# Performance work log

Hardware: AMD Instinct MI355X
Metric: run time of the kernel (lower is better)

The kernel has to match this reference:

```python
import jax, jax.numpy as jnp
import numpy as np


def setup_inputs() -> dict:
    key = jax.random.key(0)
    k1, k2, k3, k4 = jax.random.split(key, 4)
    B, Cin, Cout, K, Wd, H, Wsp = 16, 256, 256, 3, 256, 64, 64
    fan_in = Cin * K * K
    return {
        "x": jax.random.normal(k1, (B, Cin, H, Wsp), dtype=jnp.float32),
        "w": jax.random.normal(k2, (B, Wd), dtype=jnp.float32),
        "conv_weight": jax.random.normal(k3, (Cout, Cin, K, K), dtype=jnp.float32) * 0.05,
        "style_w": jax.random.normal(k4, (Cin, Wd), dtype=jnp.float32) * 0.05,
        "style_b": jnp.zeros((Cin,), dtype=jnp.float32),
        "scale": jnp.asarray(1.0 / np.sqrt(fan_in), dtype=jnp.float32),
    }


def reference(x, w, conv_weight, style_w, style_b, scale):
    # x: [B, Cin, H, W]; w: [B, Wd]; conv_weight: [Cout, Cin, K, K]
    B, Cin, H, Wsp = x.shape
    Cout, _, K, _ = conv_weight.shape
    # style modulation: s = Linear(w) -> [B, 1, Cin, 1, 1]
    s = (w @ style_w.T + style_b).reshape(B, 1, Cin, 1, 1)
    # modulate + demodulate per-sample weights: [B, Cout, Cin, K, K]
    wt = (conv_weight * scale)[None] * s
    demod = jax.lax.rsqrt(jnp.sum(wt * wt, axis=(2, 3, 4), keepdims=True) + 1e-8)
    wt = (wt * demod).reshape(B * Cout, Cin, K, K)
    # grouped conv emulation: input [1, B*Cin, H, W], groups=B
    xr = x.reshape(1, B * Cin, H, Wsp)
    pad = 1
    out = jax.lax.conv_general_dilated(
        xr, wt,
        window_strides=(1, 1),
        padding=[(pad, pad), (pad, pad)],
        dimension_numbers=("NCHW", "OIHW", "NCHW"),
        feature_group_count=B,
    )
    return out.reshape(B, Cout, out.shape[2], out.shape[3])
```

## Files before the change

kernel.cpp:

```cpp
#include <hip/hip_runtime.h>
#include <hip/hip_bf16.h>

#define BB   16
#define CIN  256
#define COUT 256
#define WD   256
#define HH   64
#define WWS  64
#define NSP  4096
#define KW   9

typedef __attribute__((ext_vector_type(8))) short short8;
typedef __attribute__((ext_vector_type(4))) float f32x4;
typedef unsigned short ushort_t;
typedef unsigned int uint_t;

#define S_BYTES (BB*CIN*4)
#define WT_OFF (S_BYTES)
#define WT_BYTES (BB*9*COUT*CIN*2)
#define X_OFF (WT_OFF + WT_BYTES)
#define X_BYTES (BB*NSP*CIN*2)
#define ZP_OFF (X_OFF + X_BYTES)
#define ZP_BYTES 4096
#define WS_NEEDED ((size_t)(ZP_OFF + ZP_BYTES))

#define WAITVM0 asm volatile("s_waitcnt vmcnt(0)" ::: "memory")
#define WAITVM4 asm volatile("s_waitcnt vmcnt(4)" ::: "memory")

__device__ inline ushort_t f2bf(float f) {
    __hip_bfloat16 h = __float2bfloat16(f);
    return __builtin_bit_cast(ushort_t, h);
}

__device__ inline void gload_lds16(const ushort_t* g, ushort_t* l) {
    __builtin_amdgcn_global_load_lds(
        (const __attribute__((address_space(1))) void*)g,
        (__attribute__((address_space(3))) void*)l, 16, 0, 0);
}

__global__ __launch_bounds__(256)
void style_kernel(const float* __restrict__ w,
                  const float* __restrict__ style_w,
                  const float* __restrict__ style_b,
                  float* __restrict__ s) {
    const int b  = blockIdx.x;
    const int ci = threadIdx.x;
    __shared__ float wsh[WD];
    wsh[ci] = w[b * WD + ci];
    __syncthreads();
    const float* row = style_w + ci * WD;
    float acc = style_b[ci];
    #pragma unroll 4
    for (int k = 0; k < WD; ++k) acc += wsh[k] * row[k];
    s[b * CIN + ci] = acc;
}

__global__ __launch_bounds__(256)
void wt_kernel(const float* __restrict__ cw, const float* __restrict__ s,
               const float* __restrict__ scale_p, ushort_t* __restrict__ wt,
               float* __restrict__ zp) {
    const int co = blockIdx.x, b = blockIdx.y, ci = threadIdx.x;
    if (co == 0 && b == 0)
        ((float4*)zp)[ci] = make_float4(0.f, 0.f, 0.f, 0.f);
    const float sv = s[b * CIN + ci] * scale_p[0];
    const float* cp = cw + ((size_t)co * CIN + ci) * KW;
    float v[9];
    float ss = 0.f;
    #pragma unroll
    for (int t = 0; t < 9; ++t) { v[t] = cp[t] * sv; ss += v[t] * v[t]; }
    #pragma unroll
    for (int off = 32; off > 0; off >>= 1) ss += __shfl_down(ss, off);
    __shared__ float red[4];
    if ((ci & 63) == 0) red[ci >> 6] = ss;
    __syncthreads();
    const float dm = rsqrtf(red[0] + red[1] + red[2] + red[3] + 1e-8f);
    #pragma unroll
    for (int t = 0; t < 9; ++t)
        wt[((size_t)(b * 9 + t) * COUT + co) * CIN + ci] = f2bf(v[t] * dm);
}

__global__ __launch_bounds__(256)
void xpose_kernel(const float* __restrict__ x, ushort_t* __restrict__ xo) {
    const int spt = blockIdx.x;
    const int cit = blockIdx.y;
    const int b   = blockIdx.z;
    const int t   = threadIdx.x;
    __shared__ ushort_t tile[64 * 72];
    const int sp0 = spt * 64, ci0 = cit * 64;
    {
        const int spq = t & 15, cil = t >> 4;
        #pragma unroll
        for (int i = 0; i < 4; ++i) {
            const int ci = cil + i * 16;
            const float4 v = *(const float4*)(x + ((size_t)(b * CIN + ci0 + ci)) * NSP + sp0 + spq * 4);
            tile[(spq * 4 + 0) * 72 + ci] = f2bf(v.x);
            tile[(spq * 4 + 1) * 72 + ci] = f2bf(v.y);
            tile[(spq * 4 + 2) * 72 + ci] = f2bf(v.z);
            tile[(spq * 4 + 3) * 72 + ci] = f2bf(v.w);
        }
    }
    __syncthreads();
    {
        const int g8 = t & 7, sp = t >> 3;
        #pragma unroll
        for (int i = 0; i < 2; ++i) {
            const int spp = sp + i * 32;
            uint4 v = *(const uint4*)&tile[spp * 72 + g8 * 8];
            *(uint4*)(xo + ((size_t)(b * NSP + sp0 + spp)) * CIN + ci0 + g8 * 8) = v;
        }
    }
}

__global__ __launch_bounds__(512, 2)
void conv_mfma_kernel(const ushort_t* __restrict__ wt,
                      const ushort_t* __restrict__ xo,
                      const ushort_t* __restrict__ zp,
                      float* __restrict__ out) {
    const int wg    = blockIdx.x;
    const int b     = (wg & 7) | (((wg >> 3) & 1) << 3);
    const int ntile = wg >> 4;
    const int y0    = ntile * 4;

    const int tid  = threadIdx.x;
    const int lane = tid & 63;
    const int w    = tid >> 6;
    const int wm   = w >> 1;
    const int wn   = w & 1;
    const int wn2  = wn * 2;
    const int l15  = lane & 15;
    const int lg   = lane >> 4;

    __shared__ __align__(16) ushort_t lds_x[6 * 66 * 128];

    const ushort_t* pa = wt + (size_t)b * (9 * COUT * CIN)
                       + (uint_t)(wm * 64 + l15) * CIN + (uint_t)(lg * 8);

    const ushort_t* xob = xo + (size_t)b * (NSP * CIN);

    f32x4 acc[4][8];
    #pragma unroll
    for (int mi = 0; mi < 4; ++mi)
        #pragma unroll
        for (int ni = 0; ni < 8; ++ni) acc[mi][ni] = (f32x4){0.f, 0.f, 0.f, 0.f};

    short8 af[2][4];

    if (tid < 192) {
        const int r = tid / 32, rem = tid % 32;
        const int c = (rem & 1) * 65, q2 = rem >> 1;
        *(uint4*)&lds_x[r * 8448 + c * 128 + q2 * 8] = make_uint4(0, 0, 0, 0);
    }

    #define STAGE_X(hh)                                                        \
    {   _Pragma("unroll")                                                      \
        for (int i_ = 0; i_ < 12; ++i_) {                                      \
            const int id_ = w + 8 * i_;                                        \
            const int r_  = id_ >> 4;                                \
            const int cg_ = id_ & 15;                             \
            const int y_  = y0 - 1 + r_;                                       \
            const int colIdx_ = 1 + cg_ * 4 + (lane >> 4);                     \
            const int sq_ = (lane & 15) ^ (colIdx_ & 15);                      \
            const ushort_t* src_ = (y_ >= 0 && y_ < HH)                        \
                ? (xob + (uint_t)(y_ * WWS + cg_ * 4 + (lane >> 4)) * CIN      \
                       + (hh) * 128 + sq_ * 8)                                 \
                : (zp + (lane & 15) * 8);                                      \
            gload_lds16(src_, lds_x + r_ * 8448 + (1 + cg_ * 4) * 128          \
                              + lane * 8);                                     \
        }                                                                      \
    }

    STAGE_X(0);
    #pragma unroll
    for (int mi = 0; mi < 4; ++mi)
        af[0][mi] = *(const short8*)(pa + mi * 4096);
    #pragma unroll
    for (int mi = 0; mi < 4; ++mi)
        af[1][mi] = *(const short8*)(pa + 65536 + mi * 4096);

    WAITVM0;
    asm volatile("s_waitcnt lgkmcnt(0)" ::: "memory");
    __builtin_amdgcn_sched_barrier(0);
    __builtin_amdgcn_s_barrier();

    #define TAP(t, CHPAR, cgv, xcb)                                            \
    {                                                                          \
        WAITVM4;                          \
        __builtin_amdgcn_sched_barrier(0);                                     \
        const int ky_ = (t) / 3, kx_ = (t) % 3;                                \
        const int P_  = ((CHPAR) + (t)) & 1;                                   \
        const ushort_t* bq_ = lds_x + (wn2 + ky_) * 8448 + xcb[kx_];           \
        short8 bf_[8];                                                         \
        _Pragma("unroll")                                                      \
        for (int ni_ = 0; ni_ < 8; ++ni_)                                      \
            bf_[ni_] = *(const short8*)(bq_ + (ni_ >> 2) * 8448                \
                                        + (ni_ & 3) * 2048);                   \
        __builtin_amdgcn_s_setprio(1);                                         \
        _Pragma("unroll")                                                      \
        for (int mi_ = 0; mi_ < 4; ++mi_)                                      \
            _Pragma("unroll")                                                  \
            for (int ni_ = 0; ni_ < 8; ++ni_)                                  \
                acc[mi_][ni_] = __builtin_amdgcn_mfma_f32_16x16x32_bf16(       \
                    bf_[ni_], af[P_][mi_], acc[mi_][ni_], 0, 0, 0);            \
        __builtin_amdgcn_s_setprio(0);                                         \
        __builtin_amdgcn_sched_barrier(0);                                     \
        {                        \
            const int t2_  = ((t) + 2) % 9;                                    \
            const int cg2_ = ((cgv) + (((t) + 2) / 9)) & 7;                    \
            const ushort_t* ap_ = pa + t2_ * 65536 + cg2_ * 32;                \
            _Pragma("unroll")                                                  \
            for (int mi_ = 0; mi_ < 4; ++mi_)                                  \
                af[P_][mi_] = *(const short8*)(ap_ + mi_ * 4096);              \
        }                                                                      \
        __builtin_amdgcn_sched_barrier(0);                                     \
    }

    #define CHUNK9(CHPAR, cgv, clv)                                            \
    {   int xcb[3];                                                            \
        _Pragma("unroll")                                                      \
        for (int kx_ = 0; kx_ < 3; ++kx_) {                                    \
            const int pos_ = ((clv) * 4 + lg) ^ ((l15 + kx_) & 15);            \
            xcb[kx_] = (l15 + kx_) * 128 + pos_ * 8;                           \
        }                                                                      \
        TAP(0, CHPAR, cgv, xcb) TAP(1, CHPAR, cgv, xcb)                        \
        TAP(2, CHPAR, cgv, xcb) TAP(3, CHPAR, cgv, xcb)                        \
        TAP(4, CHPAR, cgv, xcb) TAP(5, CHPAR, cgv, xcb)                        \
        TAP(6, CHPAR, cgv, xcb) TAP(7, CHPAR, cgv, xcb)                        \
        TAP(8, CHPAR, cgv, xcb)                                                \
    }

    #pragma unroll 1
    for (int h = 0; h < 2; ++h) {
        if (h) {
            asm volatile("s_waitcnt lgkmcnt(0)" ::: "memory");
            __builtin_amdgcn_sched_barrier(0);
            __builtin_amdgcn_s_barrier();
            STAGE_X(1);
            WAITVM0;
            __builtin_amdgcn_sched_barrier(0);
            __builtin_amdgcn_s_barrier();
        }
        #pragma unroll 1
        for (int c2 = 0; c2 < 2; ++c2) {
            const int cl0 = c2 * 2;
            const int cg0 = h * 4 + cl0;
            CHUNK9(0, cg0, cl0)
            const int cl1 = c2 * 2 + 1;
            const int cg1 = h * 4 + cl1;
            CHUNK9(1, cg1, cl1)
        }
    }
    #undef TAP
    #undef CHUNK9
    #undef STAGE_X

    asm volatile("s_waitcnt vmcnt(0) lgkmcnt(0)" ::: "memory");
    __builtin_amdgcn_sched_barrier(0);

    #pragma unroll
    for (int mi = 0; mi < 4; ++mi) {
        const int co = wm * 64 + mi * 16 + l15;
        float* ob = out + ((size_t)(b * COUT + co)) * NSP
                  + ntile * 256 + wn * 128 + lg * 4;
        #pragma unroll
        for (int ni = 0; ni < 8; ++ni)
            *(f32x4*)(ob + (ni >> 2) * 64 + (ni & 3) * 16) = acc[mi][ni];
    }
}

__global__ __launch_bounds__(256)
void modconv_kernel(const float* __restrict__ x,
                    const float* __restrict__ cw,
                    const float* __restrict__ s,
                    const float* __restrict__ scale_p,
                    float* __restrict__ out) {
    const int tile = blockIdx.x;
    const int co   = blockIdx.y;
    const int b    = blockIdx.z;
    const int tid  = threadIdx.x;
    const float scale = scale_p[0];

    __shared__ float s_wt[CIN * KW];
    __shared__ float s_x[18 * 66];
    __shared__ float red[4];

    const float* cwb = cw + (size_t)co * CIN * KW;
    const float* sb  = s + b * CIN;
    float sumsq = 0.f;
    for (int i = tid; i < CIN * KW; i += 256) {
        float v = cwb[i] * scale * sb[i / KW];
        s_wt[i] = v;
        sumsq += v * v;
    }
    #pragma unroll
    for (int off = 32; off > 0; off >>= 1) sumsq += __shfl_down(sumsq, off);
    if ((tid & 63) == 0) red[tid >> 6] = sumsq;
    __syncthreads();
    const float demod = rsqrtf(red[0] + red[1] + red[2] + red[3] + 1e-8f);
    for (int i = tid; i < CIN * KW; i += 256) s_wt[i] *= demod;

    const int tx = tid & 63;
    const int tr = tid >> 6;
    const int y0 = tile * 16;
    float acc[4] = {0.f, 0.f, 0.f, 0.f};

    for (int ci = 0; ci < CIN; ++ci) {
        __syncthreads();
        const float* xb = x + ((size_t)(b * CIN + ci)) * (HH * WWS);
        for (int idx = tid; idx < 18 * 66; idx += 256) {
            const int r = idx / 66, c = idx % 66;
            const int yg = y0 - 1 + r, xg = c - 1;
            float v = 0.f;
            if (yg >= 0 && yg < HH && xg >= 0 && xg < WWS) v = xb[yg * WWS + xg];
            s_x[idx] = v;
        }
        __syncthreads();
        const float* wr = s_wt + ci * KW;
        const float w0 = wr[0], w1 = wr[1], w2 = wr[2];
        const float w3 = wr[3], w4 = wr[4], w5 = wr[5];
        const float w6 = wr[6], w7 = wr[7], w8 = wr[8];
        const int rbase = tr * 4;
        float xv[6][3];
        #pragma unroll
        for (int j = 0; j < 6; ++j)
            #pragma unroll
            for (int k = 0; k < 3; ++k) xv[j][k] = s_x[(rbase + j) * 66 + tx + k];
        #pragma unroll
        for (int i = 0; i < 4; ++i)
            acc[i] += w0 * xv[i][0] + w1 * xv[i][1] + w2 * xv[i][2]
                    + w3 * xv[i+1][0] + w4 * xv[i+1][1] + w5 * xv[i+1][2]
                    + w6 * xv[i+2][0] + w7 * xv[i+2][1] + w8 * xv[i+2][2];
    }
    float* ob = out + (((size_t)(b * COUT + co)) * HH + y0) * WWS + tx;
    #pragma unroll
    for (int i = 0; i < 4; ++i) ob[(tr * 4 + i) * WWS] = acc[i];
}

extern "C" void kernel_launch(void* const* d_in, const int* in_sizes, int n_in,
                              void* d_out, int out_size, void* d_ws, size_t ws_size,
                              hipStream_t stream) {
    const float* x       = (const float*)d_in[0];
    const float* w       = (const float*)d_in[1];
    const float* cw      = (const float*)d_in[2];
    const float* style_w = (const float*)d_in[3];
    const float* style_b = (const float*)d_in[4];
    const float* scale_p = (const float*)d_in[5];
    float*       out     = (float*)d_out;

    float*    s    = (float*)d_ws;
    ushort_t* wswt = (ushort_t*)((char*)d_ws + WT_OFF);
    ushort_t* wsx  = (ushort_t*)((char*)d_ws + X_OFF);
    float*    zp   = (float*)((char*)d_ws + ZP_OFF);

    style_kernel<<<dim3(BB), 256, 0, stream>>>(w, style_w, style_b, s);

    if (ws_size >= WS_NEEDED) {
        wt_kernel<<<dim3(COUT, BB), 256, 0, stream>>>(cw, s, scale_p, wswt, zp);
        xpose_kernel<<<dim3(64, 4, BB), 256, 0, stream>>>(x, wsx);
        conv_mfma_kernel<<<dim3(256), 512, 0, stream>>>(wswt, wsx,
                                                        (const ushort_t*)zp, out);
    } else {
        modconv_kernel<<<dim3(4, COUT, BB), 256, 0, stream>>>(x, cw, s, scale_p, out);
    }
}
```

Before: 130.3 us.

## Split conv workgroups across output-channel halves with smaller 64-channel LDS tiles

Each conv workgroup now covers half the output channels with 256 threads instead of all 256 channels with 512 threads. The grid doubles to 512 blocks. The input tile is staged in four 64-channel quarters instead of two 128-channel halves, which halves LDS use and allows more resident blocks per CU. The cost is that every input tile is now loaded twice, once per channel half, and there are more staging barriers per block.

```diff
diff --git a/kernel.cpp b/kernel.cpp
--- a/kernel.cpp
+++ b/kernel.cpp
@@ -111,15 +111,16 @@
     }
 }
 
-__global__ __launch_bounds__(512, 2)
+__global__ __launch_bounds__(256, 2)
 void conv_mfma_kernel(const ushort_t* __restrict__ wt,
                       const ushort_t* __restrict__ xo,
                       const ushort_t* __restrict__ zp,
                       float* __restrict__ out) {
-    const int wg    = blockIdx.x;
-    const int b     = (wg & 7) | (((wg >> 3) & 1) << 3);
-    const int ntile = wg >> 4;
-    const int y0    = ntile * 4;
+    const int wg     = blockIdx.x;
+    const int b      = (wg & 7) | (((wg >> 3) & 1) << 3);
+    const int cohalf = (wg >> 4) & 1;
+    const int ntile  = wg >> 5;
+    const int y0     = ntile * 4;
 
     const int tid  = threadIdx.x;
     const int lane = tid & 63;
@@ -130,11 +131,11 @@
     const int l15  = lane & 15;
     const int lg   = lane >> 4;
 
-    __shared__ __align__(16) ushort_t lds_x[6 * 66 * 128];
+    __shared__ __align__(16) ushort_t lds_x[6 * 66 * 64];
 
     const ushort_t* pa = wt + (size_t)b * (9 * COUT * CIN)
-                       + (uint_t)(wm * 64 + l15) * CIN + (uint_t)(lg * 8);
-
+                       + (uint_t)(cohalf * 128 + wm * 64 + l15) * CIN
+                       + (uint_t)(lg * 8);
     const ushort_t* xob = xo + (size_t)b * (NSP * CIN);
 
     f32x4 acc[4][8];
@@ -145,55 +146,42 @@
 
     short8 af[2][4];
 
-    if (tid < 192) {
-        const int r = tid / 32, rem = tid % 32;
-        const int c = (rem & 1) * 65, q2 = rem >> 1;
-        *(uint4*)&lds_x[r * 8448 + c * 128 + q2 * 8] = make_uint4(0, 0, 0, 0);
-    }
-
-    #define STAGE_X(hh)                                                        \
+    if (tid < 96) {
+        const int cell = tid >> 3;
+        const int r = cell >> 1, c = (cell & 1) * 65;
+        *(uint4*)&lds_x[(r * 66 + c) * 64 + (tid & 7) * 8] =
+            make_uint4(0, 0, 0, 0);
+    }
+
+    #define STAGE_X(qt)                                                        \
     {   _Pragma("unroll")                                                      \
         for (int i_ = 0; i_ < 12; ++i_) {                                      \
-            const int id_ = w + 8 * i_;                                        \
-            const int r_  = id_ >> 4;                                \
-            const int cg_ = id_ & 15;                             \
+            const int cell_ = i_ * 4 + w;                           \
+            const int r_  = cell_ >> 3;                              \
+            const int c0_ = 1 + (cell_ & 7) * 8;                               \
             const int y_  = y0 - 1 + r_;                                       \
-            const int colIdx_ = 1 + cg_ * 4 + (lane >> 4);                     \
-            const int sq_ = (lane & 15) ^ (colIdx_ & 15);                      \
+            const int c_  = c0_ + (lane >> 3);                                 \
+            const int qq_ = (lane & 7) ^ (c_ & 7);                             \
             const ushort_t* src_ = (y_ >= 0 && y_ < HH)                        \
-                ? (xob + (uint_t)(y_ * WWS + cg_ * 4 + (lane >> 4)) * CIN      \
-                       + (hh) * 128 + sq_ * 8)                                 \
-                : (zp + (lane & 15) * 8);                                      \
-            gload_lds16(src_, lds_x + r_ * 8448 + (1 + cg_ * 4) * 128          \
-                              + lane * 8);                                     \
+                ? (xob + (uint_t)(y_ * WWS + c_ - 1) * CIN + (qt) * 64         \
+                       + qq_ * 8)                                              \
+                : (zp + lane * 8);                                             \
+            gload_lds16(src_, lds_x + (r_ * 66 + c0_) * 64 + lane * 8);        \
         }                                                                      \
     }
 
-    STAGE_X(0);
-    #pragma unroll
-    for (int mi = 0; mi < 4; ++mi)
-        af[0][mi] = *(const short8*)(pa + mi * 4096);
-    #pragma unroll
-    for (int mi = 0; mi < 4; ++mi)
-        af[1][mi] = *(const short8*)(pa + 65536 + mi * 4096);
-
-    WAITVM0;
-    asm volatile("s_waitcnt lgkmcnt(0)" ::: "memory");
-    __builtin_amdgcn_sched_barrier(0);
-    __builtin_amdgcn_s_barrier();
-
-    #define TAP(t, CHPAR, cgv, xcb)                                            \
+    #define TAPB(ch2, t, BX, PAQ, PAQN)                                        \
     {                                                                          \
-        WAITVM4;                          \
+        constexpr int u_ = (ch2) * 9 + (t);                                    \
+        constexpr int P_ = u_ & 1;                                             \
+        WAITVM4;                                                               \
         __builtin_amdgcn_sched_barrier(0);                                     \
-        const int ky_ = (t) / 3, kx_ = (t) % 3;                                \
-        const int P_  = ((CHPAR) + (t)) & 1;                                   \
-        const ushort_t* bq_ = lds_x + (wn2 + ky_) * 8448 + xcb[kx_];           \
+        constexpr int ky_ = (t) / 3, kx_ = (t) % 3;                            \
         short8 bf_[8];                                                         \
         _Pragma("unroll")                                                      \
         for (int ni_ = 0; ni_ < 8; ++ni_)                                      \
-            bf_[ni_] = *(const short8*)(bq_ + (ni_ >> 2) * 8448                \
-                                        + (ni_ & 3) * 2048);                   \
+            bf_[ni_] = *(const short8*)(lds_x + BX[kx_]                        \
+                        + (((ni_ >> 2) + ky_) * 66) * 64 + (ni_ & 3) * 1024);  \
         __builtin_amdgcn_s_setprio(1);                                         \
         _Pragma("unroll")                                                      \
         for (int mi_ = 0; mi_ < 4; ++mi_)                                      \
@@ -204,9 +192,15 @@
         __builtin_amdgcn_s_setprio(0);                                         \
         __builtin_amdgcn_sched_barrier(0);                                     \
         {                        \
-            const int t2_  = ((t) + 2) % 9;                                    \
-            const int cg2_ = ((cgv) + (((t) + 2) / 9)) & 7;                    \
-            const ushort_t* ap_ = pa + t2_ * 65536 + cg2_ * 32;                \
+            const ushort_t* ap_;                                               \
+            if constexpr (u_ + 2 < 18) {                                       \
+                constexpr int tap2_ = (u_ + 2) % 9;                            \
+                constexpr int cgo_  = (u_ + 2) / 9;                            \
+                ap_ = (PAQ) + tap2_ * 65536 + cgo_ * 32;                       \
+            } else {                                                           \
+                constexpr int tap2_ = u_ - 16;                                 \
+                ap_ = (PAQN) + tap2_ * 65536;                                  \
+            }                                                                  \
             _Pragma("unroll")                                                  \
             for (int mi_ = 0; mi_ < 4; ++mi_)                                  \
                 af[P_][mi_] = *(const short8*)(ap_ + mi_ * 4096);              \
@@ -214,43 +208,49 @@
         __builtin_amdgcn_sched_barrier(0);                                     \
     }
 
-    #define CHUNK9(CHPAR, cgv, clv)                                            \
-    {   int xcb[3];                                                            \
-        _Pragma("unroll")                                                      \
-        for (int kx_ = 0; kx_ < 3; ++kx_) {                                    \
-            const int pos_ = ((clv) * 4 + lg) ^ ((l15 + kx_) & 15);            \
-            xcb[kx_] = (l15 + kx_) * 128 + pos_ * 8;                           \
-        }                                                                      \
-        TAP(0, CHPAR, cgv, xcb) TAP(1, CHPAR, cgv, xcb)                        \
-        TAP(2, CHPAR, cgv, xcb) TAP(3, CHPAR, cgv, xcb)                        \
-        TAP(4, CHPAR, cgv, xcb) TAP(5, CHPAR, cgv, xcb)                        \
-        TAP(6, CHPAR, cgv, xcb) TAP(7, CHPAR, cgv, xcb)                        \
-        TAP(8, CHPAR, cgv, xcb)                                                \
-    }
+    STAGE_X(0);
+    #pragma unroll
+    for (int mi = 0; mi < 4; ++mi)
+        af[0][mi] = *(const short8*)(pa + mi * 4096);
+    #pragma unroll
+    for (int mi = 0; mi < 4; ++mi)
+        af[1][mi] = *(const short8*)(pa + 65536 + mi * 4096);
+    WAITVM0;
+    asm volatile("s_waitcnt lgkmcnt(0)" ::: "memory");
+    __builtin_amdgcn_sched_barrier(0);
+    __builtin_amdgcn_s_barrier();
 
     #pragma unroll 1
-    for (int h = 0; h < 2; ++h) {
-        if (h) {
+    for (int qt = 0; qt < 4; ++qt) {
+        if (qt) {
             asm volatile("s_waitcnt lgkmcnt(0)" ::: "memory");
             __builtin_amdgcn_sched_barrier(0);
             __builtin_amdgcn_s_barrier();
-            STAGE_X(1);
+            STAGE_X(qt);
             WAITVM0;
             __builtin_amdgcn_sched_barrier(0);
             __builtin_amdgcn_s_barrier();
         }
-        #pragma unroll 1
-        for (int c2 = 0; c2 < 2; ++c2) {
-            const int cl0 = c2 * 2;
-            const int cg0 = h * 4 + cl0;
-            CHUNK9(0, cg0, cl0)
-            const int cl1 = c2 * 2 + 1;
-            const int cg1 = h * 4 + cl1;
-            CHUNK9(1, cg1, cl1)
-        }
-    }
-    #undef TAP
-    #undef CHUNK9
+        const ushort_t* paq  = pa + qt * 64;
+        const ushort_t* paqn = pa + ((qt + 1) & 3) * 64;
+
+        int bx0[3], bx1[3];
+        #pragma unroll
+        for (int kx = 0; kx < 3; ++kx) {
+            const int colb = (wn2 * 66 + l15 + kx) * 64;
+            const int k7   = (l15 + kx) & 7;
+            bx0[kx] = colb + ((0 + lg) ^ k7) * 8;
+            bx1[kx] = colb + ((4 + lg) ^ k7) * 8;
+        }
+
+        TAPB(0,0,bx0,paq,paqn) TAPB(0,1,bx0,paq,paqn) TAPB(0,2,bx0,paq,paqn)
+        TAPB(0,3,bx0,paq,paqn) TAPB(0,4,bx0,paq,paqn) TAPB(0,5,bx0,paq,paqn)
+        TAPB(0,6,bx0,paq,paqn) TAPB(0,7,bx0,paq,paqn) TAPB(0,8,bx0,paq,paqn)
+        TAPB(1,0,bx1,paq,paqn) TAPB(1,1,bx1,paq,paqn) TAPB(1,2,bx1,paq,paqn)
+        TAPB(1,3,bx1,paq,paqn) TAPB(1,4,bx1,paq,paqn) TAPB(1,5,bx1,paq,paqn)
+        TAPB(1,6,bx1,paq,paqn) TAPB(1,7,bx1,paq,paqn) TAPB(1,8,bx1,paq,paqn)
+    }
+    #undef TAPB
     #undef STAGE_X
 
     asm volatile("s_waitcnt vmcnt(0) lgkmcnt(0)" ::: "memory");
@@ -258,7 +258,7 @@
 
     #pragma unroll
     for (int mi = 0; mi < 4; ++mi) {
-        const int co = wm * 64 + mi * 16 + l15;
+        const int co = cohalf * 128 + wm * 64 + mi * 16 + l15;
         float* ob = out + ((size_t)(b * COUT + co)) * NSP
                   + ntile * 256 + wn * 128 + lg * 4;
         #pragma unroll
@@ -356,7 +356,7 @@
     if (ws_size >= WS_NEEDED) {
         wt_kernel<<<dim3(COUT, BB), 256, 0, stream>>>(cw, s, scale_p, wswt, zp);
         xpose_kernel<<<dim3(64, 4, BB), 256, 0, stream>>>(x, wsx);
-        conv_mfma_kernel<<<dim3(256), 512, 0, stream>>>(wswt, wsx,
+        conv_mfma_kernel<<<dim3(512), 256, 0, stream>>>(wswt, wsx,
                                                         (const ushort_t*)zp, out);
     } else {
         modconv_kernel<<<dim3(4, COUT, BB), 256, 0, stream>>>(x, cw, s, scale_p, out);
```

Result: slower. 144.2 us (+10.6%).
